# Optimization experiments

Hardware: AMD Instinct MI355X
Metric: run time of the kernel (lower is better)

## Reference

```python
import jax, jax.numpy as jnp
import numpy as np
from jax import lax


def setup_inputs() -> dict:
    key = jax.random.key(0)
    ks = jax.random.split(key, 11)
    B, S, V, E, H = 32, 256, 32000, 128, 128
    return {
        "sequence": jax.random.randint(ks[0], (B, S), 0, V),
        "encoder_output": jax.random.normal(ks[1], (B, S, H), jnp.float32),
        "encoder_output_hidden": jax.random.normal(ks[2], (1, B, H), jnp.float32),
        "encoder_output_cell": jax.random.normal(ks[3], (1, B, H), jnp.float32),
        "emb": jax.random.normal(ks[4], (V, E), jnp.float32) * 0.02,
        "W_ih": jax.random.normal(ks[5], (4 * H, E + H), jnp.float32) * 0.05,
        "b_ih": jax.random.normal(ks[6], (4 * H,), jnp.float32) * 0.05,
        "W_hh": jax.random.normal(ks[7], (4 * H, H), jnp.float32) * 0.05,
        "b_hh": jax.random.normal(ks[8], (4 * H,), jnp.float32) * 0.05,
        "W_pred": jax.random.normal(ks[9], (V, H), jnp.float32) * 0.05,
        "b_pred": jax.random.normal(ks[10], (V,), jnp.float32) * 0.05,
    }


def reference(sequence, encoder_output, encoder_output_hidden, encoder_output_cell,
              emb, W_ih, b_ih, W_hh, b_hh, W_pred, b_pred):
    B, S = sequence.shape
    H = W_hh.shape[1]
    x = emb[sequence]                      # [B, S, E]
    h0 = encoder_output_hidden[0]          # [B, H] fixed state fed every step
    c0 = encoder_output_cell[0]            # [B, H]
    # gate contribution from the fixed hidden state is constant over time
    hh = h0 @ W_hh.T + b_hh                # [B, 4H]

    def step(h_prev, x_t):
        inp = jnp.concatenate([x_t, h_prev], axis=1)   # [B, E+H]
        gates = inp @ W_ih.T + b_ih + hh               # [B, 4H]
        i, f, g, o = jnp.split(gates, 4, axis=1)       # torch LSTMCell order
        c = jax.nn.sigmoid(f) * c0 + jax.nn.sigmoid(i) * jnp.tanh(g)
        h = jax.nn.sigmoid(o) * jnp.tanh(c)
        return h, h

    h_init = jnp.zeros((B, H), x.dtype)
    _, hs = lax.scan(step, h_init, jnp.swapaxes(x, 0, 1))  # hs: [S, B, H]
    hs = jnp.swapaxes(hs, 0, 1)                            # [B, S, H]
    logits = hs @ W_pred.T + b_pred                        # [B, S, V]
    return jax.nn.log_softmax(logits, axis=-1)
```

## Files before the change

### kernel.cpp

```cpp
#include <hip/hip_runtime.h>

typedef short bf16x8 __attribute__((ext_vector_type(8)));
typedef float f32x4  __attribute__((ext_vector_type(4)));
typedef unsigned short u16;
typedef unsigned short u16x8 __attribute__((ext_vector_type(8)));

#define NB   32
#define NS   256
#define NV   32000
#define NE   128
#define NH   128
#define NR   8192
#define NG   512
#define NCHUNK 500

__device__ __forceinline__ float sigm(float x){
    return __builtin_amdgcn_rcpf(1.0f + __expf(-x));
}
__device__ __forceinline__ float tanh_fast(float x){
    return 1.0f - 2.0f*__builtin_amdgcn_rcpf(1.0f + __expf(2.0f*x));
}

__device__ __forceinline__ u16 f2bf(float x){
    unsigned u = __float_as_uint(x);
    unsigned r = (u + 0x7FFFu + ((u >> 16) & 1u)) >> 16;
    return (u16)r;
}

__device__ __forceinline__ void lds_barrier(){
    asm volatile("s_waitcnt lgkmcnt(0)" ::: "memory");
    __builtin_amdgcn_s_barrier();
    __builtin_amdgcn_sched_barrier(0);
}


__global__ __launch_bounds__(256) void khh(const float* __restrict__ h0,
                                           const float* __restrict__ W_hh,
                                           const float* __restrict__ b_ih,
                                           const float* __restrict__ b_hh,
                                           float* __restrict__ hh){
    int idx = blockIdx.x*256 + threadIdx.x;
    int b = idx >> 9, j = idx & 511;
    const float4* h4 = (const float4*)(h0 + b*NH);
    const float4* w4 = (const float4*)(W_hh + j*NH);
    float acc = b_ih[j] + b_hh[j];
    #pragma unroll
    for (int k = 0; k < 32; ++k){
        float4 a = h4[k], w = w4[k];
        acc += a.x*w.x + a.y*w.y + a.z*w.z + a.w*w.w;
    }
    hh[idx] = acc;
}

__global__ __launch_bounds__(256) void kwb(const float* __restrict__ src, u16* __restrict__ dst){
    int a8 = blockIdx.x*256 + threadIdx.x;
    int a = a8 * 8;
    int rb = a >> 13; int blk = (a >> 9) & 15; int lane = (a >> 3) & 63;
    int q = blk & 3, kk = blk >> 2;
    int l15 = lane & 15, l4 = lane >> 4;
    int m = rb*64 + q*16 + l15;
    int j = kk*32 + l4*8;
    const float* s = src + (size_t)m*NH + j;
    float4 x = *(const float4*)s, y = *(const float4*)(s + 4);
    u16x8 o;
    o[0]=f2bf(x.x); o[1]=f2bf(x.y); o[2]=f2bf(x.z); o[3]=f2bf(x.w);
    o[4]=f2bf(y.x); o[5]=f2bf(y.y); o[6]=f2bf(y.z); o[7]=f2bf(y.w);
    *(u16x8*)&dst[a] = o;
}

__global__ __launch_bounds__(256) void ktr(const u16* __restrict__ src, u16* __restrict__ dst){
    int a8 = blockIdx.x*256 + threadIdx.x;
    int a = a8 * 8;
    int rb = a >> 13; int blk = (a >> 9) & 15; int lane = (a >> 3) & 63;
    int q = blk & 3, kk = blk >> 2;
    int l15 = lane & 15, l4 = lane >> 4;
    int m = rb*64 + q*16 + l15;
    int j = kk*32 + l4*8;
    *(uint4*)&dst[a] = *(const uint4*)&src[(size_t)m*NH + j];
}

__global__ __launch_bounds__(256) void kxg(const int* __restrict__ seq,
                                           const float* __restrict__ emb,
                                           const float* __restrict__ W_ih,
                                           float* __restrict__ xg){
    __shared__ float4 xs[16][32];
    int m0 = blockIdx.x * 16;
    int t = threadIdx.x;
    int r = t >> 4, k4 = t & 15;
    int tok = seq[m0 + r];
    xs[r][k4]      = *(const float4*)(emb + (size_t)tok*NE + k4*4);
    xs[r][k4 + 16] = *(const float4*)(emb + (size_t)tok*NE + (k4+16)*4);
    __syncthreads();
    int j0 = t, j1 = t + 256;
    const float4* w0 = (const float4*)(W_ih + (size_t)j0*256);
    const float4* w1 = (const float4*)(W_ih + (size_t)j1*256);
    float acc0[16], acc1[16];
    #pragma unroll
    for (int r2 = 0; r2 < 16; ++r2){ acc0[r2]=0.f; acc1[r2]=0.f; }
    #pragma unroll
    for (int k = 0; k < 32; ++k){
        float4 wa = w0[k], wb = w1[k];
        #pragma unroll
        for (int r2 = 0; r2 < 16; ++r2){
            float4 xv = xs[r2][k];
            acc0[r2] += xv.x*wa.x + xv.y*wa.y + xv.z*wa.z + xv.w*wa.w;
            acc1[r2] += xv.x*wb.x + xv.y*wb.y + xv.z*wb.z + xv.w*wb.w;
        }
    }
    #pragma unroll
    for (int r2 = 0; r2 < 16; ++r2){
        xg[(size_t)(m0+r2)*NG + j0] = acc0[r2];
        xg[(size_t)(m0+r2)*NG + j1] = acc1[r2];
    }
}

#define DOT16(ACC, B) {                                                         \
    asm("v_dot2_f32_bf16 %0, %1, %2, %0" : "+v"(ACC) : "v"(hq0.x), "v"(w2[(B)+0])); \
    asm("v_dot2_f32_bf16 %0, %1, %2, %0" : "+v"(ACC) : "v"(hq0.y), "v"(w2[(B)+1])); \
    asm("v_dot2_f32_bf16 %0, %1, %2, %0" : "+v"(ACC) : "v"(hq0.z), "v"(w2[(B)+2])); \
    asm("v_dot2_f32_bf16 %0, %1, %2, %0" : "+v"(ACC) : "v"(hq0.w), "v"(w2[(B)+3])); \
    asm("v_dot2_f32_bf16 %0, %1, %2, %0" : "+v"(ACC) : "v"(hq1.x), "v"(w2[(B)+4])); \
    asm("v_dot2_f32_bf16 %0, %1, %2, %0" : "+v"(ACC) : "v"(hq1.y), "v"(w2[(B)+5])); \
    asm("v_dot2_f32_bf16 %0, %1, %2, %0" : "+v"(ACC) : "v"(hq1.z), "v"(w2[(B)+6])); \
    asm("v_dot2_f32_bf16 %0, %1, %2, %0" : "+v"(ACC) : "v"(hq1.w), "v"(w2[(B)+7])); \
    asm("v_dot2_f32_bf16 %0, %1, %2, %0" : "+v"(ACC) : "v"(hq2.x), "v"(w2[(B)+8])); \
    asm("v_dot2_f32_bf16 %0, %1, %2, %0" : "+v"(ACC) : "v"(hq2.y), "v"(w2[(B)+9])); \
    asm("v_dot2_f32_bf16 %0, %1, %2, %0" : "+v"(ACC) : "v"(hq2.z), "v"(w2[(B)+10])); \
    asm("v_dot2_f32_bf16 %0, %1, %2, %0" : "+v"(ACC) : "v"(hq2.w), "v"(w2[(B)+11])); \
    asm("v_dot2_f32_bf16 %0, %1, %2, %0" : "+v"(ACC) : "v"(hq3.x), "v"(w2[(B)+12])); \
    asm("v_dot2_f32_bf16 %0, %1, %2, %0" : "+v"(ACC) : "v"(hq3.y), "v"(w2[(B)+13])); \
    asm("v_dot2_f32_bf16 %0, %1, %2, %0" : "+v"(ACC) : "v"(hq3.z), "v"(w2[(B)+14])); \
    asm("v_dot2_f32_bf16 %0, %1, %2, %0" : "+v"(ACC) : "v"(hq3.w), "v"(w2[(B)+15])); \
}

#define LSTM_STEP(S, XV) {                                                      \
    const uint4* h4 = (const uint4*)&hsh2[(S) & 1][0];                          \
    uint4 hq0 = h4[p4+0], hq1 = h4[p4+1], hq2 = h4[p4+2], hq3 = h4[p4+3];       \
    float s0=0.f, s1=0.f, s2=0.f, s3=0.f;                                       \
    DOT16(s0, 0); DOT16(s1, 16); DOT16(s2, 32); DOT16(s3, 48);                  \
    float hbx = hba + (XV);                                                     \
    s0 += (p == 0) ? hbx : 0.f;                                                 \
    s1 += (p == 1) ? hbx : 0.f;                                                 \
    s2 += (p == 2) ? hbx : 0.f;                                                 \
    s3 += (p == 3) ? hbx : 0.f;                                                 \
    s0 += __shfl_xor(s0, 1); s0 += __shfl_xor(s0, 2);                           \
    s1 += __shfl_xor(s1, 1); s1 += __shfl_xor(s1, 2);                           \
    s2 += __shfl_xor(s2, 1); s2 += __shfl_xor(s2, 2);                           \
    s3 += __shfl_xor(s3, 1); s3 += __shfl_xor(s3, 2);                           \
    float cc = sigm(s1)*c0r + sigm(s0)*tanh_fast(s2);                           \
    float h  = sigm(s3)*tanh_fast(cc);                                          \
    u16 hb16 = f2bf(h);                                                         \
    unsigned hp = __shfl_xor((unsigned)hb16, 4);              \
    if ((t & 7) == 0){                                                          \
        unsigned pair = (hp << 16) | (unsigned)hb16;                            \
        hsh2[((S) & 1) ^ 1][r >> 1] = pair;                                     \
        *(unsigned*)&hrow[(S)*NH + r] = pair;                                   \
    }                                                                           \
    lds_barrier();                                                              \
}

__global__ __launch_bounds__(512, 1) void klstm(const float* __restrict__ xg,
                                                const float* __restrict__ hh,
                                                const float* __restrict__ W_ih,
                                                const float* __restrict__ c0,
                                                u16* __restrict__ hs){
    __shared__ __align__(16) unsigned hsh2[2][64];
    int b = blockIdx.x, t = threadIdx.x;
    int r = t >> 2;
    int p = t & 3;
    int p4 = p * 4;
    unsigned w2[64];
    #pragma unroll
    for (int j = 0; j < 4; ++j){
        const float2* wrj = (const float2*)(W_ih + (size_t)(j*NH + r)*256 + 128 + p*32);
        #pragma unroll
        for (int k = 0; k < 16; ++k){
            float2 v = wrj[k];
            w2[j*16 + k] = ((unsigned)f2bf(v.y) << 16) | (unsigned)f2bf(v.x);
        }
    }
    float hba = hh[b*NG + p*NH + r];
    float c0r = c0[b*NH + r];
    if (t < 64){ hsh2[0][t] = 0u; }
    __syncthreads();
    const float* xrow = xg + (size_t)b*NS*NG + p*NH + r;
    u16* hrow = hs + (size_t)b*NS*NH;
    float xv0 = xrow[0], xv1 = xrow[NG], xv2 = xrow[2*NG], xv3 = xrow[3*NG];
    for (int s4 = 0; s4 < NS; s4 += 4){
        float n0=0.f, n1=0.f, n2=0.f, n3=0.f;
        if (s4 + 4 < NS){
            const float* xn = xrow + (size_t)(s4+4)*NG;
            n0 = xn[0]; n1 = xn[NG]; n2 = xn[2*NG]; n3 = xn[3*NG];
        }
        LSTM_STEP(s4+0, xv0);
        LSTM_STEP(s4+1, xv1);
        LSTM_STEP(s4+2, xv2);
        LSTM_STEP(s4+3, xv3);
        xv0=n0; xv1=n1; xv2=n2; xv3=n3;
    }
}


#define LOAD_A(DST, R) {                                                        \
    int rbA = (mbase >> 6) + (R)*2 + wr;                                        \
    const u16* pa = hsbF + (size_t)rbA*8192 + lane*8;                           \
    _Pragma("unroll")                                                           \
    for (int q = 0; q < 4; ++q)                                                 \
        _Pragma("unroll")                                                       \
        for (int kk = 0; kk < 4; ++kk)                                          \
            DST[q][kk] = *(const bf16x8*)&pa[(kk*4 + q)*512];                   \
}

template<int PASS>
__global__ __launch_bounds__(256, 2) void kgemm(const u16* __restrict__ hsbF,
                                                const u16* __restrict__ wbF,
                                                const float* __restrict__ bpred,
                                                const float* __restrict__ lse,
                                                float* __restrict__ psum,
                                                float* __restrict__ out){
    int tid = threadIdx.x;
    int bid = blockIdx.x;
    int c    = bid >> 1;
    int half = bid & 1;
    int n0 = c * 128;
    int mbase = half * 4096;

    int wid = tid >> 6, lane = tid & 63;
    int wr = wid >> 1, wc = wid & 1;
    int l15 = lane & 15, l4 = lane >> 4;
    const float L2E = 1.44269504f;
    float4 bp4[4];
    #pragma unroll
    for (int f = 0; f < 4; ++f){
        bp4[f] = *(const float4*)&bpred[n0 + wc*64 + f*16 + l4*4];
        if (PASS == 0){
            bp4[f].x *= L2E; bp4[f].y *= L2E; bp4[f].z *= L2E; bp4[f].w *= L2E;
        }
    }

    bf16x8 bfr[4][4];
    {
        int rbB = c*2 + wc;
        const u16* pb = wbF + (size_t)rbB*8192 + lane*8;
        #pragma unroll
        for (int f = 0; f < 4; ++f)
            #pragma unroll
            for (int kk = 0; kk < 4; ++kk)
                bfr[f][kk] = *(const bf16x8*)&pb[(kk*4 + f)*512];
    }

    bf16x8 af[4][4];
    LOAD_A(af, 0);
    for (int r = 0; r < 32; ++r){
        f32x4 acc[4][4];
        #pragma unroll
        for (int q = 0; q < 4; ++q)
            #pragma unroll
            for (int f = 0; f < 4; ++f)
                acc[q][f] = (f32x4){0.f,0.f,0.f,0.f};
        #pragma unroll
        for (int f = 0; f < 4; ++f)
            #pragma unroll
            for (int q = 0; q < 4; ++q)
                #pragma unroll
                for (int kk = 0; kk < 4; ++kk)
                    acc[q][f] = __builtin_amdgcn_mfma_f32_16x16x32_bf16(
                        bfr[f][kk], af[q][kk], acc[q][f], 0, 0, 0);

        if (r + 1 < 32) LOAD_A(af, r+1);

        if (PASS == 0){
            float lsum[4];
            #pragma unroll
            for (int q = 0; q < 4; ++q){
                float s = 0.f;
                #pragma unroll
                for (int f = 0; f < 4; ++f)
                    #pragma unroll
                    for (int rr = 0; rr < 4; ++rr){
                        float tt = fmaf(acc[q][f][rr], L2E, bp4[f][rr]);
                        float e; asm("v_exp_f32 %0, %1" : "=v"(e) : "v"(tt));
                        s += e;
                    }
                s += __shfl_xor(s, 16);
                s += __shfl_xor(s, 32);
                lsum[q] = s;
            }
            float sv = (l4 == 0) ? lsum[0] : (l4 == 1) ? lsum[1]
                     : (l4 == 2) ? lsum[2] : lsum[3];
            psum[(size_t)(c*2 + wc)*NR + mbase + r*128 + wr*64 + lane] = sv;
        } else {
            #pragma unroll
            for (int q = 0; q < 4; ++q){
                int grow = mbase + r*128 + wr*64 + q*16 + l15;
                float lw = lse[grow];
                float* orow = out + (size_t)grow*NV + n0 + wc*64 + l4*4;
                #pragma unroll
                for (int f = 0; f < 4; ++f){
                    f32x4 v;
                    v[0] = acc[q][f][0] + bp4[f].x - lw;
                    v[1] = acc[q][f][1] + bp4[f].y - lw;
                    v[2] = acc[q][f][2] + bp4[f].z - lw;
                    v[3] = acc[q][f][3] + bp4[f].w - lw;
                    *(f32x4*)&orow[f*16] = v;
                }
            }
        }
    }
}

__global__ __launch_bounds__(256) void klse(const float* __restrict__ psum,
                                            float* __restrict__ lse){
    __shared__ float red[32][8];
    int t = threadIdx.x;
    int row = blockIdx.x*32 + (t >> 3);
    int grp = t & 7;
    float S = 0.f;
    for (int cc = grp; cc < NCHUNK; cc += 8)
        S += psum[(size_t)cc*NR + row];
    red[t >> 3][grp] = S;
    __syncthreads();
    if (grp == 0){
        float s2 = 0.f;
        #pragma unroll
        for (int g = 0; g < 8; ++g) s2 += red[t >> 3][g];
        lse[row] = __logf(s2);
    }
}

extern "C" void kernel_launch(void* const* d_in, const int* in_sizes, int n_in,
                              void* d_out, int out_size, void* d_ws, size_t ws_size,
                              hipStream_t stream){
    (void)in_sizes; (void)n_in; (void)out_size; (void)ws_size;
    const int*   seq    = (const int*)d_in[0];
    const float* h0     = (const float*)d_in[2];
    const float* c0     = (const float*)d_in[3];
    const float* emb    = (const float*)d_in[4];
    const float* W_ih   = (const float*)d_in[5];
    const float* b_ih   = (const float*)d_in[6];
    const float* W_hh   = (const float*)d_in[7];
    const float* b_hh   = (const float*)d_in[8];
    const float* W_pred = (const float*)d_in[9];
    const float* b_pred = (const float*)d_in[10];
    float* out = (float*)d_out;

    char* ws = (char*)d_ws;
    float* xg   = (float*)(ws);
    float* psum = (float*)(ws);
    float* hh   = (float*)(ws + 16777216);
    u16*   hsb  = (u16*)  (ws + 16842752);
    u16*   wbbF = (u16*)  (ws + 18939904);
    float* lse  = (float*)(ws + 27131904);
    u16*   hsbF = (u16*)  (ws + 27164672);

    khh<<<64, 256, 0, stream>>>(h0, W_hh, b_ih, b_hh, hh);
    kwb<<<2000, 256, 0, stream>>>(W_pred, wbbF);
    kxg<<<512, 256, 0, stream>>>(seq, emb, W_ih, xg);
    klstm<<<32, 512, 0, stream>>>(xg, hh, W_ih, c0, hsb);
    ktr<<<1024, 256, 0, stream>>>(hsb, hsbF);
    kgemm<0><<<500, 256, 0, stream>>>(hsbF, wbbF, b_pred, nullptr, psum, out);
    klse<<<256, 256, 0, stream>>>(psum, lse);
    kgemm<1><<<500, 256, 0, stream>>>(hsbF, wbbF, b_pred, lse, psum, out);
}
```

Before: 554.6 us.

## Make LM-head GEMM hold activations resident and stream vocab chunks across blocks

Result: slower. 582.7 us (+5.1%).

```diff
diff --git a/kernel.cpp b/kernel.cpp
--- a/kernel.cpp
+++ b/kernel.cpp
@@ -83,32 +83,33 @@
                                            const float* __restrict__ emb,
                                            const float* __restrict__ W_ih,
                                            float* __restrict__ xg){
-    __shared__ float4 xs[16][32];
-    int m0 = blockIdx.x * 16;
+    __shared__ float4 xs[32][32];
+    int m0 = blockIdx.x * 32;
     int t = threadIdx.x;
-    int r = t >> 4, k4 = t & 15;
+    int r = t >> 3, k8 = t & 7;
     int tok = seq[m0 + r];
-    xs[r][k4]      = *(const float4*)(emb + (size_t)tok*NE + k4*4);
-    xs[r][k4 + 16] = *(const float4*)(emb + (size_t)tok*NE + (k4+16)*4);
+    #pragma unroll
+    for (int j = 0; j < 4; ++j)
+        xs[r][k8*4 + j] = *(const float4*)(emb + (size_t)tok*NE + (k8*4 + j)*4);
     __syncthreads();
     int j0 = t, j1 = t + 256;
     const float4* w0 = (const float4*)(W_ih + (size_t)j0*256);
     const float4* w1 = (const float4*)(W_ih + (size_t)j1*256);
-    float acc0[16], acc1[16];
-    #pragma unroll
-    for (int r2 = 0; r2 < 16; ++r2){ acc0[r2]=0.f; acc1[r2]=0.f; }
+    float acc0[32], acc1[32];
+    #pragma unroll
+    for (int r2 = 0; r2 < 32; ++r2){ acc0[r2]=0.f; acc1[r2]=0.f; }
     #pragma unroll
     for (int k = 0; k < 32; ++k){
         float4 wa = w0[k], wb = w1[k];
         #pragma unroll
-        for (int r2 = 0; r2 < 16; ++r2){
+        for (int r2 = 0; r2 < 32; ++r2){
             float4 xv = xs[r2][k];
             acc0[r2] += xv.x*wa.x + xv.y*wa.y + xv.z*wa.z + xv.w*wa.w;
             acc1[r2] += xv.x*wb.x + xv.y*wb.y + xv.z*wb.z + xv.w*wb.w;
         }
     }
     #pragma unroll
-    for (int r2 = 0; r2 < 16; ++r2){
+    for (int r2 = 0; r2 < 32; ++r2){
         xg[(size_t)(m0+r2)*NG + j0] = acc0[r2];
         xg[(size_t)(m0+r2)*NG + j1] = acc1[r2];
     }
@@ -201,14 +202,13 @@
 }
 
 
-#define LOAD_A(DST, R) {                                                        \
-    int rbA = (mbase >> 6) + (R)*2 + wr;                                        \
-    const u16* pa = hsbF + (size_t)rbA*8192 + lane*8;                           \
+#define LOAD_B(CH) {                                                            \
+    const u16* pb = wbF + (size_t)(CH)*8192 + lane*8;                           \
     _Pragma("unroll")                                                           \
-    for (int q = 0; q < 4; ++q)                                                 \
+    for (int f = 0; f < 4; ++f)                                                 \
         _Pragma("unroll")                                                       \
         for (int kk = 0; kk < 4; ++kk)                                          \
-            DST[q][kk] = *(const bf16x8*)&pa[(kk*4 + q)*512];                   \
+            bfr[f][kk] = *(const bf16x8*)&pb[(kk*4 + f)*512];                   \
 }
 
 template<int PASS>
@@ -220,38 +220,42 @@
                                                 float* __restrict__ out){
     int tid = threadIdx.x;
     int bid = blockIdx.x;
-    int c    = bid >> 1;
-    int half = bid & 1;
-    int n0 = c * 128;
-    int mbase = half * 4096;
-
+    int rg = bid / 50;
+    int cg = bid % 50;
     int wid = tid >> 6, lane = tid & 63;
-    int wr = wid >> 1, wc = wid & 1;
     int l15 = lane & 15, l4 = lane >> 4;
+    int rbA = rg*4 + wid;
     const float L2E = 1.44269504f;
-    float4 bp4[4];
-    #pragma unroll
-    for (int f = 0; f < 4; ++f){
-        bp4[f] = *(const float4*)&bpred[n0 + wc*64 + f*16 + l4*4];
-        if (PASS == 0){
-            bp4[f].x *= L2E; bp4[f].y *= L2E; bp4[f].z *= L2E; bp4[f].w *= L2E;
-        }
+
+    bf16x8 af[4][4];
+    {
+        const u16* pa = hsbF + (size_t)rbA*8192 + lane*8;
+        #pragma unroll
+        for (int q = 0; q < 4; ++q)
+            #pragma unroll
+            for (int kk = 0; kk < 4; ++kk)
+                af[q][kk] = *(const bf16x8*)&pa[(kk*4 + q)*512];
+    }
+    float lw[4];
+    if (PASS == 1){
+        #pragma unroll
+        for (int q = 0; q < 4; ++q)
+            lw[q] = lse[rbA*64 + q*16 + l15];
     }
 
     bf16x8 bfr[4][4];
-    {
-        int rbB = c*2 + wc;
-        const u16* pb = wbF + (size_t)rbB*8192 + lane*8;
-        #pragma unroll
-        for (int f = 0; f < 4; ++f)
-            #pragma unroll
-            for (int kk = 0; kk < 4; ++kk)
-                bfr[f][kk] = *(const bf16x8*)&pb[(kk*4 + f)*512];
-    }
-
-    bf16x8 af[4][4];
-    LOAD_A(af, 0);
-    for (int r = 0; r < 32; ++r){
+    LOAD_B(cg*10);
+    for (int i = 0; i < 10; ++i){
+        int ch = cg*10 + i;
+        int n0 = ch*64;
+        float4 bp4[4];
+        #pragma unroll
+        for (int f = 0; f < 4; ++f){
+            bp4[f] = *(const float4*)&bpred[n0 + f*16 + l4*4];
+            if (PASS == 0){
+                bp4[f].x *= L2E; bp4[f].y *= L2E; bp4[f].z *= L2E; bp4[f].w *= L2E;
+            }
+        }
         f32x4 acc[4][4];
         #pragma unroll
         for (int q = 0; q < 4; ++q)
@@ -267,7 +271,7 @@
                     acc[q][f] = __builtin_amdgcn_mfma_f32_16x16x32_bf16(
                         bfr[f][kk], af[q][kk], acc[q][f], 0, 0, 0);
 
-        if (r + 1 < 32) LOAD_A(af, r+1);
+        if (i + 1 < 10) LOAD_B(ch + 1);
 
         if (PASS == 0){
             float lsum[4];
@@ -288,20 +292,19 @@
             }
             float sv = (l4 == 0) ? lsum[0] : (l4 == 1) ? lsum[1]
                      : (l4 == 2) ? lsum[2] : lsum[3];
-            psum[(size_t)(c*2 + wc)*NR + mbase + r*128 + wr*64 + lane] = sv;
+            psum[(size_t)ch*NR + rbA*64 + lane] = sv;
         } else {
             #pragma unroll
             for (int q = 0; q < 4; ++q){
-                int grow = mbase + r*128 + wr*64 + q*16 + l15;
-                float lw = lse[grow];
-                float* orow = out + (size_t)grow*NV + n0 + wc*64 + l4*4;
+                int grow = rbA*64 + q*16 + l15;
+                float* orow = out + (size_t)grow*NV + n0 + l4*4;
                 #pragma unroll
                 for (int f = 0; f < 4; ++f){
                     f32x4 v;
-                    v[0] = acc[q][f][0] + bp4[f].x - lw;
-                    v[1] = acc[q][f][1] + bp4[f].y - lw;
-                    v[2] = acc[q][f][2] + bp4[f].z - lw;
-                    v[3] = acc[q][f][3] + bp4[f].w - lw;
+                    v[0] = acc[q][f][0] + bp4[f].x - lw[q];
+                    v[1] = acc[q][f][1] + bp4[f].y - lw[q];
+                    v[2] = acc[q][f][2] + bp4[f].z - lw[q];
+                    v[3] = acc[q][f][3] + bp4[f].w - lw[q];
                     *(f32x4*)&orow[f*16] = v;
                 }
             }
@@ -355,10 +358,10 @@
 
     khh<<<64, 256, 0, stream>>>(h0, W_hh, b_ih, b_hh, hh);
     kwb<<<2000, 256, 0, stream>>>(W_pred, wbbF);
-    kxg<<<512, 256, 0, stream>>>(seq, emb, W_ih, xg);
+    kxg<<<256, 256, 0, stream>>>(seq, emb, W_ih, xg);
     klstm<<<32, 512, 0, stream>>>(xg, hh, W_ih, c0, hsb);
     ktr<<<1024, 256, 0, stream>>>(hsb, hsbF);
-    kgemm<0><<<500, 256, 0, stream>>>(hsbF, wbbF, b_pred, nullptr, psum, out);
+    kgemm<0><<<1600, 256, 0, stream>>>(hsbF, wbbF, b_pred, nullptr, psum, out);
     klse<<<256, 256, 0, stream>>>(psum, lse);
-    kgemm<1><<<500, 256, 0, stream>>>(hsbF, wbbF, b_pred, lse, psum, out);
-}
+    kgemm<1><<<1600, 256, 0, stream>>>(hsbF, wbbF, b_pred, lse, psum, out);
+}
```
